# Kernel tuning notes

Hardware: AMD Instinct MI355X
Metric: run time of the kernel (lower is better)

Reference implementation:

```python
import jax, jax.numpy as jnp
import numpy as np

L1, L2, ALPHA, BETA, EPS = 0.5, 1.5, 1.0, 50000000.0, 1e-08


def tube(att, label):
    # per-row cosine/sine TUBE distance, fully vectorized over batch
    dot = jnp.sum(att * label, axis=-1)            # [B]
    p_norm = jnp.sqrt(jnp.sum(att * att, axis=-1))
    g_norm = jnp.sqrt(jnp.sum(label * label, axis=-1))
    denom = p_norm * g_norm
    cosine = jnp.where(denom == 0, 0.0, dot / jnp.where(denom == 0, 1.0, denom))
    s_s = 1.0 - jnp.square(cosine)
    # s_s < 0 -> sine = 0 ; s_s == 0 -> sqrt(s_s + eps) ; else sqrt(s_s)
    sine = jnp.where(s_s < 0, 0.0, jnp.sqrt(jnp.where(s_s <= 0, EPS, s_s)))
    r_all = p_norm * cosine / jnp.where(g_norm == 0, g_norm + EPS, g_norm)
    base = p_norm * sine + jnp.abs(g_norm - p_norm * cosine)
    ds = jnp.where(r_all >= 1, L1 * base,
         jnp.where(r_all >= 0, base,
                   L2 * jnp.abs(p_norm * cosine - g_norm - p_norm * sine)))
    ds = -jnp.log(jnp.tanh(1.0 / ds))
    return jnp.mean(ds)


def kl_loss(mu, logvar):
    return -0.5 * BETA * jnp.mean(1.0 + logvar - jnp.square(mu) - jnp.exp(logvar))


def cross_entropy(logits, label_idx):
    logp = jax.nn.log_softmax(logits, axis=-1)
    return -jnp.mean(jnp.take_along_axis(logp, label_idx[:, None], axis=1)[:, 0])


def setup_inputs() -> dict:
    key = jax.random.key(0)
    ks = jax.random.split(key, 12)
    B, C, D, Z = 16384, 100, 512, 128
    return {
        "fusion_out": jax.random.normal(ks[0], (B, C), jnp.float32),
        "comple_out": jax.random.normal(ks[1], (B, D), jnp.float32),
        "labels": jax.random.normal(ks[2], (B, C), jnp.float32),
        "labels_encoder": jax.random.normal(ks[3], (B, D), jnp.float32),
        "x_A": jax.random.normal(ks[4], (B, D), jnp.float32),
        "x_A_reconstructed": jax.random.normal(ks[5], (B, D), jnp.float32),
        "x_B": jax.random.normal(ks[6], (B, D), jnp.float32),
        "x_B_reconstructed": jax.random.normal(ks[7], (B, D), jnp.float32),
        "x_C": jax.random.normal(ks[8], (B, D), jnp.float32),
        "x_C_reconstructed": jax.random.normal(ks[9], (B, D), jnp.float32),
        "mu": jax.random.normal(ks[10], (B, Z), jnp.float32),
        "logvar": jax.random.normal(ks[11], (B, Z), jnp.float32),
    }


def reference(fusion_out, comple_out, labels, labels_encoder, x_A,
              x_A_reconstructed, x_B, x_B_reconstructed, x_C,
              x_C_reconstructed, mu, logvar):
    label_idx = jnp.argmax(labels, axis=1)
    tube_A = ALPHA * tube(x_A_reconstructed, x_A)
    tube_B = ALPHA * tube(x_B_reconstructed, x_B)
    tube_C = ALPHA * tube(x_C_reconstructed, x_C)
    kl = kl_loss(mu, logvar)
    st_all = ALPHA * tube(comple_out, labels_encoder)
    ce = cross_entropy(fusion_out, label_idx)
    return tube_A + tube_B + tube_C + kl + ce + st_all
```

## Files before the change

kernel.cpp:

```cpp
#include <hip/hip_runtime.h>
#include <math.h>

static constexpr float kL1   = 0.5f;
static constexpr float kL2   = 1.5f;
static constexpr float kBeta = 50000000.0f;
static constexpr float kEps  = 1e-08f;

__device__ __forceinline__ float waveSum(float v) {
#pragma unroll
    for (int off = 32; off > 0; off >>= 1) v += __shfl_xor(v, off, 64);
    return v;
}

__device__ __forceinline__ float tubeTail(float dot, float pp, float gg) {
    float p_norm = sqrtf(pp);
    float g_norm = sqrtf(gg);
    float denom  = p_norm * g_norm;
    float cosine = (denom == 0.0f) ? 0.0f : dot / denom;
    float s_s    = 1.0f - cosine * cosine;
    float sine   = (s_s < 0.0f) ? 0.0f : sqrtf((s_s <= 0.0f) ? kEps : s_s);
    float gd     = (g_norm == 0.0f) ? (g_norm + kEps) : g_norm;
    float pc     = p_norm * cosine;
    float r_all  = pc / gd;
    float base   = p_norm * sine + fabsf(g_norm - pc);
    float ds     = (r_all >= 1.0f) ? (kL1 * base)
                 : ((r_all >= 0.0f) ? base
                                    : kL2 * fabsf(pc - g_norm - p_norm * sine));
    float t  = 1.0f / ds;
    float em = __expf(-2.0f * t);
    return __logf(1.0f + em) - __logf(fmaxf(1.0f - em, 1e-30f));
}

__global__ __launch_bounds__(256) void fused_loss_partials(
    const float* __restrict__ fusion_out, const float* __restrict__ comple_out,
    const float* __restrict__ labels,     const float* __restrict__ labels_enc,
    const float* __restrict__ xA,  const float* __restrict__ xAr,
    const float* __restrict__ xB,  const float* __restrict__ xBr,
    const float* __restrict__ xC,  const float* __restrict__ xCr,
    const float* __restrict__ mu,  const float* __restrict__ logvar,
    float* __restrict__ partials,
    int B, int C, int Z,
    int tubeBlocks, int klBlocks, int ceBlocks)
{
    const int lane = threadIdx.x & 63;
    const int wave = threadIdx.x >> 6;
    const int wavesPerBlock = blockDim.x >> 6;
    const int bid = blockIdx.x;
    const int D = 512;

    float my = 0.0f;

    if (bid < tubeBlocks) {
        const int globalWave = bid * wavesPerBlock + wave;
        const int totalWaves = tubeBlocks * wavesPerBlock;
        const int totalRows  = 4 * B;
        const float* atts[4] = { xAr, xBr, xCr, comple_out };
        const float* labs[4] = { xA,  xB,  xC,  labels_enc  };
        float acc = 0.0f;
        for (int row = globalWave; row < totalRows; row += 2 * totalWaves) {
            const int row2 = row + totalWaves;
            const int p0 = row  >> 14, r0 = row  & (B - 1);
            const int p1 = row2 >> 14, r1 = row2 & (B - 1);
            const float4* a0 = (const float4*)(atts[p0] + (size_t)r0 * D);
            const float4* l0 = (const float4*)(labs[p0] + (size_t)r0 * D);
            const float4* a1 = (const float4*)(atts[p1] + (size_t)r1 * D);
            const float4* l1 = (const float4*)(labs[p1] + (size_t)r1 * D);
            float4 A0 = a0[lane], A1 = a0[lane + 64];
            float4 L0 = l0[lane], L1 = l0[lane + 64];
            float4 A2 = a1[lane], A3 = a1[lane + 64];
            float4 L2 = l1[lane], L3 = l1[lane + 64];
            float dotA = A0.x*L0.x + A0.y*L0.y + A0.z*L0.z + A0.w*L0.w
                       + A1.x*L1.x + A1.y*L1.y + A1.z*L1.z + A1.w*L1.w;
            float ppA  = A0.x*A0.x + A0.y*A0.y + A0.z*A0.z + A0.w*A0.w
                       + A1.x*A1.x + A1.y*A1.y + A1.z*A1.z + A1.w*A1.w;
            float ggA  = L0.x*L0.x + L0.y*L0.y + L0.z*L0.z + L0.w*L0.w
                       + L1.x*L1.x + L1.y*L1.y + L1.z*L1.z + L1.w*L1.w;
            float dotB = A2.x*L2.x + A2.y*L2.y + A2.z*L2.z + A2.w*L2.w
                       + A3.x*L3.x + A3.y*L3.y + A3.z*L3.z + A3.w*L3.w;
            float ppB  = A2.x*A2.x + A2.y*A2.y + A2.z*A2.z + A2.w*A2.w
                       + A3.x*A3.x + A3.y*A3.y + A3.z*A3.z + A3.w*A3.w;
            float ggB  = L2.x*L2.x + L2.y*L2.y + L2.z*L2.z + L2.w*L2.w
                       + L3.x*L3.x + L3.y*L3.y + L3.z*L3.z + L3.w*L3.w;
#pragma unroll
            for (int off = 32; off > 0; off >>= 1) {
                dotA += __shfl_xor(dotA, off, 64);
                ppA  += __shfl_xor(ppA,  off, 64);
                ggA  += __shfl_xor(ggA,  off, 64);
                dotB += __shfl_xor(dotB, off, 64);
                ppB  += __shfl_xor(ppB,  off, 64);
                ggB  += __shfl_xor(ggB,  off, 64);
            }
            if (lane == 0) {
                acc += tubeTail(dotA, ppA, ggA);
                acc += tubeTail(dotB, ppB, ggB);
            }
        }
        my = acc / (float)B;
    } else if (bid < tubeBlocks + klBlocks) {
        const int b2 = bid - tubeBlocks;
        const int n4 = (B * Z) >> 2;
        const float4* mu4 = (const float4*)mu;
        const float4* lv4 = (const float4*)logvar;
        const int tid    = b2 * blockDim.x + threadIdx.x;
        const int stride = klBlocks * blockDim.x;
        float acc = 0.0f;
        for (int i = tid; i < n4; i += stride) {
            float4 m = mu4[i];
            float4 l = lv4[i];
            acc += (1.0f + l.x - m.x * m.x - __expf(l.x));
            acc += (1.0f + l.y - m.y * m.y - __expf(l.y));
            acc += (1.0f + l.z - m.z * m.z - __expf(l.z));
            acc += (1.0f + l.w - m.w * m.w - __expf(l.w));
        }
        my = acc * (-0.5f * kBeta / (float)(B * Z));
    } else {
        const int b3 = bid - tubeBlocks - klBlocks;
        const int globalWave = b3 * wavesPerBlock + wave;
        const int totalWaves = ceBlocks * wavesPerBlock;
        float acc = 0.0f;
        for (int r = globalWave; r < B; r += totalWaves) {
            const float* lrow = labels     + (size_t)r * C;
            const float* frow = fusion_out + (size_t)r * C;
            const bool has0 = (lane < C);
            const bool has1 = (lane + 64 < C);
            float v0 = has0 ? lrow[lane]      : -INFINITY;
            float v1 = has1 ? lrow[lane + 64] : -INFINITY;
            float f0 = has0 ? frow[lane]      : -INFINITY;
            float f1 = has1 ? frow[lane + 64] : -INFINITY;
            float bv; int bi;
            if (v1 > v0) { bv = v1; bi = lane + 64; } else { bv = v0; bi = lane; }
#pragma unroll
            for (int off = 32; off > 0; off >>= 1) {
                float ov = __shfl_xor(bv, off, 64);
                int   oi = __shfl_xor(bi, off, 64);
                if (ov > bv || (ov == bv && oi < bi)) { bv = ov; bi = oi; }
            }
            float m = fmaxf(f0, f1);
#pragma unroll
            for (int off = 32; off > 0; off >>= 1) m = fmaxf(m, __shfl_xor(m, off, 64));
            float e = 0.0f;
            if (has0) e += __expf(f0 - m);
            if (has1) e += __expf(f1 - m);
            e = waveSum(e);
            float t = (bi < 64) ? __shfl(f0, bi, 64) : __shfl(f1, bi - 64, 64);
            if (lane == 0) acc += -(t - m - __logf(e));
        }
        my = acc / (float)B;
    }

    float s = waveSum(my);
    __shared__ float sw[8];
    if (lane == 0) sw[wave] = s;
    __syncthreads();
    if (threadIdx.x == 0) {
        float tot = 0.0f;
        for (int i = 0; i < wavesPerBlock; ++i) tot += sw[i];
        partials[bid] = tot;
    }
}

__global__ __launch_bounds__(256) void reduce_partials(
    const float* __restrict__ partials, float* __restrict__ out, int n)
{
    float s = 0.0f;
    for (int i = threadIdx.x; i < n; i += 256) s += partials[i];
    s = waveSum(s);
    __shared__ float sw[4];
    const int lane = threadIdx.x & 63;
    const int wave = threadIdx.x >> 6;
    if (lane == 0) sw[wave] = s;
    __syncthreads();
    if (threadIdx.x == 0) out[0] = sw[0] + sw[1] + sw[2] + sw[3];
}

extern "C" void kernel_launch(void* const* d_in, const int* in_sizes, int n_in,
                              void* d_out, int out_size, void* d_ws, size_t ws_size,
                              hipStream_t stream) {
    const float* fusion_out = (const float*)d_in[0];
    const float* comple_out = (const float*)d_in[1];
    const float* labels     = (const float*)d_in[2];
    const float* labels_enc = (const float*)d_in[3];
    const float* xA  = (const float*)d_in[4];
    const float* xAr = (const float*)d_in[5];
    const float* xB  = (const float*)d_in[6];
    const float* xBr = (const float*)d_in[7];
    const float* xC  = (const float*)d_in[8];
    const float* xCr = (const float*)d_in[9];
    const float* mu  = (const float*)d_in[10];
    const float* lv  = (const float*)d_in[11];
    float* out = (float*)d_out;
    float* ws  = (float*)d_ws;

    const int B = 16384;
    const int C = in_sizes[0] / B;
    const int Z = in_sizes[10] / B;

    const int tubeBlocks = 4096;
    const int klBlocks   = 512;
    const int ceBlocks   = 2048;
    const int totalBlocks = tubeBlocks + klBlocks + ceBlocks;

    fused_loss_partials<<<totalBlocks, 256, 0, stream>>>(
        fusion_out, comple_out, labels, labels_enc,
        xA, xAr, xB, xBr, xC, xCr, mu, lv,
        ws, B, C, Z, tubeBlocks, klBlocks, ceBlocks);
    reduce_partials<<<1, 256, 0, stream>>>(ws, out, totalBlocks);
}
```

Baseline: 288.3 us.

## Merge loss phases per block, use half-wave rows, prefetch next tube row

Every block now runs all three phases (tube, KL, cross-entropy) through grid-stride loops, instead of splitting blocks by role. The grid shrinks to 2048 blocks with a launch-bounds occupancy hint. In the tube phase each half-wave handles one 512-float row, so one wave covers two rows with shorter shuffle reductions. Loads for the next row pair are issued before the current pair is reduced, to hide memory latency. The cost is more live registers, and every lane now evaluates the transcendental tail, with the 32 duplicate results cancelled by the scale factor.

```diff
diff --git a/kernel.cpp b/kernel.cpp
--- a/kernel.cpp
+++ b/kernel.cpp
@@ -31,7 +31,12 @@
     return __logf(1.0f + em) - __logf(fmaxf(1.0f - em, 1e-30f));
 }
 
-__global__ __launch_bounds__(256) void fused_loss_partials(
+#define ACC3(A, L)                                        \
+    dot += A.x*L.x + A.y*L.y + A.z*L.z + A.w*L.w;         \
+    pp  += A.x*A.x + A.y*A.y + A.z*A.z + A.w*A.w;         \
+    gg  += L.x*L.x + L.y*L.y + L.z*L.z + L.w*L.w;
+
+__global__ __launch_bounds__(256, 4) void fused_loss_partials(
     const float* __restrict__ fusion_out, const float* __restrict__ comple_out,
     const float* __restrict__ labels,     const float* __restrict__ labels_enc,
     const float* __restrict__ xA,  const float* __restrict__ xAr,
@@ -39,72 +44,75 @@
     const float* __restrict__ xC,  const float* __restrict__ xCr,
     const float* __restrict__ mu,  const float* __restrict__ logvar,
     float* __restrict__ partials,
-    int B, int C, int Z,
-    int tubeBlocks, int klBlocks, int ceBlocks)
+    int B, int C, int Z)
 {
     const int lane = threadIdx.x & 63;
     const int wave = threadIdx.x >> 6;
     const int wavesPerBlock = blockDim.x >> 6;
-    const int bid = blockIdx.x;
+    const int globalWave = blockIdx.x * wavesPerBlock + wave;
+    const int totalWaves = gridDim.x * wavesPerBlock;
     const int D = 512;
 
     float my = 0.0f;
 
-    if (bid < tubeBlocks) {
-        const int globalWave = bid * wavesPerBlock + wave;
-        const int totalWaves = tubeBlocks * wavesPerBlock;
-        const int totalRows  = 4 * B;
-        const float* atts[4] = { xAr, xBr, xCr, comple_out };
-        const float* labs[4] = { xA,  xB,  xC,  labels_enc  };
-        float acc = 0.0f;
-        for (int row = globalWave; row < totalRows; row += 2 * totalWaves) {
-            const int row2 = row + totalWaves;
-            const int p0 = row  >> 14, r0 = row  & (B - 1);
-            const int p1 = row2 >> 14, r1 = row2 & (B - 1);
-            const float4* a0 = (const float4*)(atts[p0] + (size_t)r0 * D);
-            const float4* l0 = (const float4*)(labs[p0] + (size_t)r0 * D);
-            const float4* a1 = (const float4*)(atts[p1] + (size_t)r1 * D);
-            const float4* l1 = (const float4*)(labs[p1] + (size_t)r1 * D);
-            float4 A0 = a0[lane], A1 = a0[lane + 64];
-            float4 L0 = l0[lane], L1 = l0[lane + 64];
-            float4 A2 = a1[lane], A3 = a1[lane + 64];
-            float4 L2 = l1[lane], L3 = l1[lane + 64];
-            float dotA = A0.x*L0.x + A0.y*L0.y + A0.z*L0.z + A0.w*L0.w
-                       + A1.x*L1.x + A1.y*L1.y + A1.z*L1.z + A1.w*L1.w;
-            float ppA  = A0.x*A0.x + A0.y*A0.y + A0.z*A0.z + A0.w*A0.w
-                       + A1.x*A1.x + A1.y*A1.y + A1.z*A1.z + A1.w*A1.w;
-            float ggA  = L0.x*L0.x + L0.y*L0.y + L0.z*L0.z + L0.w*L0.w
-                       + L1.x*L1.x + L1.y*L1.y + L1.z*L1.z + L1.w*L1.w;
-            float dotB = A2.x*L2.x + A2.y*L2.y + A2.z*L2.z + A2.w*L2.w
-                       + A3.x*L3.x + A3.y*L3.y + A3.z*L3.z + A3.w*L3.w;
-            float ppB  = A2.x*A2.x + A2.y*A2.y + A2.z*A2.z + A2.w*A2.w
-                       + A3.x*A3.x + A3.y*A3.y + A3.z*A3.z + A3.w*A3.w;
-            float ggB  = L2.x*L2.x + L2.y*L2.y + L2.z*L2.z + L2.w*L2.w
-                       + L3.x*L3.x + L3.y*L3.y + L3.z*L3.z + L3.w*L3.w;
-#pragma unroll
-            for (int off = 32; off > 0; off >>= 1) {
-                dotA += __shfl_xor(dotA, off, 64);
-                ppA  += __shfl_xor(ppA,  off, 64);
-                ggA  += __shfl_xor(ggA,  off, 64);
-                dotB += __shfl_xor(dotB, off, 64);
-                ppB  += __shfl_xor(ppB,  off, 64);
-                ggB  += __shfl_xor(ggB,  off, 64);
+    {
+        const int h   = lane >> 5;
+        const int sub = lane & 31;
+        const int NP  = (4 * B) >> 1;
+        const int fo  = h * 128 + sub;
+
+        float tubeAcc = 0.0f;
+
+        int t = globalWave;
+        float4 cA0, cA1, cA2, cA3, cL0, cL1, cL2, cL3;
+        if (t < NP) {
+            const int row0 = 2 * t;
+            const int p = row0 >> 14, r0 = row0 & (B - 1);
+            const float* ab = (p == 0) ? xAr : (p == 1) ? xBr : (p == 2) ? xCr : comple_out;
+            const float* lb = (p == 0) ? xA  : (p == 1) ? xB  : (p == 2) ? xC  : labels_enc;
+            const float4* a = (const float4*)(ab + (size_t)r0 * D) + fo;
+            const float4* l = (const float4*)(lb + (size_t)r0 * D) + fo;
+            cA0 = a[0]; cA1 = a[32]; cA2 = a[64]; cA3 = a[96];
+            cL0 = l[0]; cL1 = l[32]; cL2 = l[64]; cL3 = l[96];
+        }
+        for (; t < NP; t += totalWaves) {
+            int tn = t + totalWaves;
+            if (tn >= NP) tn = t;
+            const int rown = 2 * tn;
+            const int pn = rown >> 14, rn = rown & (B - 1);
+            const float* abn = (pn == 0) ? xAr : (pn == 1) ? xBr : (pn == 2) ? xCr : comple_out;
+            const float* lbn = (pn == 0) ? xA  : (pn == 1) ? xB  : (pn == 2) ? xC  : labels_enc;
+            const float4* an = (const float4*)(abn + (size_t)rn * D) + fo;
+            const float4* ln = (const float4*)(lbn + (size_t)rn * D) + fo;
+            float4 nA0 = an[0], nA1 = an[32], nA2 = an[64], nA3 = an[96];
+            float4 nL0 = ln[0], nL1 = ln[32], nL2 = ln[64], nL3 = ln[96];
+
+            float dot = 0.0f, pp = 0.0f, gg = 0.0f;
+            ACC3(cA0, cL0); ACC3(cA1, cL1); ACC3(cA2, cL2); ACC3(cA3, cL3);
+
+#pragma unroll
+            for (int off = 16; off > 0; off >>= 1) {
+                dot += __shfl_xor(dot, off, 64);
+                pp  += __shfl_xor(pp,  off, 64);
+                gg  += __shfl_xor(gg,  off, 64);
             }
-            if (lane == 0) {
-                acc += tubeTail(dotA, ppA, ggA);
-                acc += tubeTail(dotB, ppB, ggB);
-            }
-        }
-        my = acc / (float)B;
-    } else if (bid < tubeBlocks + klBlocks) {
-        const int b2 = bid - tubeBlocks;
+
+            tubeAcc += tubeTail(dot, pp, gg);
+
+            cA0 = nA0; cA1 = nA1; cA2 = nA2; cA3 = nA3;
+            cL0 = nL0; cL1 = nL1; cL2 = nL2; cL3 = nL3;
+        }
+        my += tubeAcc * (1.0f / (32.0f * (float)B));
+    }
+
+    {
         const int n4 = (B * Z) >> 2;
         const float4* mu4 = (const float4*)mu;
         const float4* lv4 = (const float4*)logvar;
-        const int tid    = b2 * blockDim.x + threadIdx.x;
-        const int stride = klBlocks * blockDim.x;
+        const int tid      = blockIdx.x * blockDim.x + threadIdx.x;
+        const int nThreads = gridDim.x * blockDim.x;
         float acc = 0.0f;
-        for (int i = tid; i < n4; i += stride) {
+        for (int i = tid; i < n4; i += nThreads) {
             float4 m = mu4[i];
             float4 l = lv4[i];
             acc += (1.0f + l.x - m.x * m.x - __expf(l.x));
@@ -112,11 +120,10 @@
             acc += (1.0f + l.z - m.z * m.z - __expf(l.z));
             acc += (1.0f + l.w - m.w * m.w - __expf(l.w));
         }
-        my = acc * (-0.5f * kBeta / (float)(B * Z));
-    } else {
-        const int b3 = bid - tubeBlocks - klBlocks;
-        const int globalWave = b3 * wavesPerBlock + wave;
-        const int totalWaves = ceBlocks * wavesPerBlock;
+        my += acc * (-0.5f * kBeta / (float)(B * Z));
+    }
+
+    {
         float acc = 0.0f;
         for (int r = globalWave; r < B; r += totalWaves) {
             const float* lrow = labels     + (size_t)r * C;
@@ -142,10 +149,10 @@
             if (has0) e += __expf(f0 - m);
             if (has1) e += __expf(f1 - m);
             e = waveSum(e);
-            float t = (bi < 64) ? __shfl(f0, bi, 64) : __shfl(f1, bi - 64, 64);
-            if (lane == 0) acc += -(t - m - __logf(e));
-        }
-        my = acc / (float)B;
+            float tgt = (bi < 64) ? __shfl(f0, bi, 64) : __shfl(f1, bi - 64, 64);
+            if (lane == 0) acc += -(tgt - m - __logf(e));
+        }
+        my += acc / (float)B;
     }
 
     float s = waveSum(my);
@@ -155,7 +162,7 @@
     if (threadIdx.x == 0) {
         float tot = 0.0f;
         for (int i = 0; i < wavesPerBlock; ++i) tot += sw[i];
-        partials[bid] = tot;
+        partials[blockIdx.x] = tot;
     }
 }
 
@@ -195,14 +202,11 @@
     const int C = in_sizes[0] / B;
     const int Z = in_sizes[10] / B;
 
-    const int tubeBlocks = 4096;
-    const int klBlocks   = 512;
-    const int ceBlocks   = 2048;
-    const int totalBlocks = tubeBlocks + klBlocks + ceBlocks;
+    const int totalBlocks = 2048;
 
     fused_loss_partials<<<totalBlocks, 256, 0, stream>>>(
         fusion_out, comple_out, labels, labels_enc,
         xA, xAr, xB, xBr, xC, xCr, mu, lv,
-        ws, B, C, Z, tubeBlocks, klBlocks, ceBlocks);
+        ws, B, C, Z);
     reduce_partials<<<1, 256, 0, stream>>>(ws, out, totalBlocks);
 }
```

New measurement: 282.6 us. 1.02x faster.
